# Optimization experiments

Hardware: AMD Instinct MI355X
Metric: run time of the kernel (lower is better)

## Reference

```python
import jax, jax.numpy as jnp
import numpy as np

N_IN = 200000
N_OUT = 600000
K = 27          # 3x3x3 kernel offsets
P = 150000      # kernel-map pairs per offset
C_IN = 96
C_OUT = 96
BN_EPS = 1e-5


def setup_inputs() -> dict:
    key = jax.random.key(0)
    k1, k2, k3, k4 = jax.random.split(key, 4)
    feats = jax.random.normal(k1, (N_IN, C_IN), dtype=jnp.float32)
    # kernel map: per offset, input-site indices and output-site indices
    in_idx = jax.random.randint(k2, (K, P), 0, N_IN, dtype=jnp.int32)
    out_idx = jax.random.randint(k3, (K, P), 0, N_OUT, dtype=jnp.int32)
    weight = jax.random.normal(k4, (K, C_IN, C_OUT), dtype=jnp.float32) * (1.0 / np.sqrt(C_IN * K))
    gamma = jnp.ones((C_OUT,), dtype=jnp.float32)
    beta = jnp.zeros((C_OUT,), dtype=jnp.float32)
    return {"feats": feats, "in_idx": in_idx, "out_idx": out_idx,
            "weight": weight, "gamma": gamma, "beta": beta}


def reference(feats, in_idx, out_idx, weight, gamma, beta):
    # Sparse transposed conv: gather -> matmul -> scatter-add per kernel offset.
    out = jnp.zeros((N_OUT, C_OUT), dtype=feats.dtype)
    for k in range(K):  # fixed small loop over kernel offsets (structurally distinct weights)
        contrib = feats[in_idx[k]] @ weight[k]          # [P, C_OUT]
        out = out.at[out_idx[k]].add(contrib)
    # BatchNorm (training-mode batch stats over active output sites), per channel
    mean = jnp.mean(out, axis=0)
    var = jnp.mean((out - mean) ** 2, axis=0)
    y = (out - mean) * jax.lax.rsqrt(var + BN_EPS) * gamma + beta
    # ReLU
    return jax.nn.relu(y)
```

## Files before the change

kernel.cpp:

```cpp
#include <hip/hip_runtime.h>
#include <hip/hip_bf16.h>

#define N_IN   200000
#define N_OUT  600000
#define KOFF   27
#define PPAIR  150000
#define NPAIR  (KOFF * PPAIR)
#define C      96
#define BN_EPS 1e-5f

using bf16x8 = __attribute__((ext_vector_type(8))) __bf16;
using f32x4  = __attribute__((ext_vector_type(4))) float;

static __device__ __forceinline__ unsigned short f2b(float x) {
    __hip_bfloat16 h = __float2bfloat16(x);
    return *reinterpret_cast<unsigned short*>(&h);
}
static __device__ __forceinline__ float b_lo(unsigned int u) { return __uint_as_float(u << 16); }
static __device__ __forceinline__ float b_hi(unsigned int u) { return __uint_as_float(u & 0xffff0000u); }

__global__ void cvt_feats(const float* __restrict__ src, unsigned short* __restrict__ dst) {
    int t = blockIdx.x * 256 + threadIdx.x;
    const float4* s4 = (const float4*)src;
    float4 a = s4[2 * t], b = s4[2 * t + 1];
    union { unsigned short u[8]; uint4 v; } r;
    r.u[0] = f2b(a.x); r.u[1] = f2b(a.y); r.u[2] = f2b(a.z); r.u[3] = f2b(a.w);
    r.u[4] = f2b(b.x); r.u[5] = f2b(b.y); r.u[6] = f2b(b.z); r.u[7] = f2b(b.w);
    ((uint4*)dst)[t] = r.v;
}

__global__ void cvt_w(const float* __restrict__ w, unsigned short* __restrict__ wt) {
    int t = blockIdx.x * 256 + threadIdx.x;
    int k = t / 9216;
    int rem = t - k * 9216;
    int o = rem / 96;
    int i = rem - o * 96;
    wt[t] = f2b(w[k * 9216 + i * 96 + o]);
}

__global__ void k_hist(const int* __restrict__ out_idx, int* __restrict__ counts,
                       int* __restrict__ lrank) {
    int t = blockIdx.x * 256 + threadIdx.x;
    if (t < NPAIR) lrank[t] = atomicAdd(&counts[out_idx[t]], 1);
}

__global__ void k_bsum(const int* __restrict__ counts, int* __restrict__ bsum) {
    __shared__ int ls[256];
    int b = blockIdx.x, t = threadIdx.x;
    int base = b * 1024 + t * 4;
    int s = 0;
#pragma unroll
    for (int j = 0; j < 4; j++) { int i = base + j; if (i < N_OUT) s += counts[i]; }
    ls[t] = s;
    __syncthreads();
    for (int off = 128; off > 0; off >>= 1) {
        if (t < off) ls[t] += ls[t + off];
        __syncthreads();
    }
    if (t == 0) bsum[b] = ls[0];
}

__global__ void k_scan_bsum(const int* __restrict__ bsum, int* __restrict__ bsum_ex) {
    __shared__ int sc[1024];
    int t = threadIdx.x;
    int v = (t < 586) ? bsum[t] : 0;
    sc[t] = v;
    __syncthreads();
    for (int off = 1; off < 1024; off <<= 1) {
        int add = (t >= off) ? sc[t - off] : 0;
        __syncthreads();
        sc[t] += add;
        __syncthreads();
    }
    bsum_ex[t] = sc[t] - v;
}

__global__ void k_scan_local(const int* __restrict__ counts, const int* __restrict__ bsum_ex,
                             int* __restrict__ csr) {
    __shared__ int sc[256];
    int b = blockIdx.x, t = threadIdx.x;
    int base = b * 1024 + t * 4;
    int c[4];
    int s = 0;
#pragma unroll
    for (int j = 0; j < 4; j++) {
        int i = base + j;
        c[j] = (i < N_OUT) ? counts[i] : 0;
        s += c[j];
    }
    sc[t] = s;
    __syncthreads();
    for (int off = 1; off < 256; off <<= 1) {
        int add = (t >= off) ? sc[t - off] : 0;
        __syncthreads();
        sc[t] += add;
        __syncthreads();
    }
    int run = bsum_ex[b] + sc[t] - s;
#pragma unroll
    for (int j = 0; j < 4; j++) {
        int i = base + j;
        if (i < N_OUT) {
            csr[i] = run;
            run += c[j];
            if (i == N_OUT - 1) csr[N_OUT] = run;
        }
    }
}

__global__ __launch_bounds__(256, 6) void contrib_k(
    const unsigned short* __restrict__ fb,
    const unsigned short* __restrict__ wt,
    const int* __restrict__ in_idx,
    const int* __restrict__ out_idx,
    const int* __restrict__ csr,
    const int* __restrict__ lrank,
    unsigned short* __restrict__ contrib)
{
    __shared__ int s_g[64];
    __shared__ int s_rank[64];

    const int t    = threadIdx.x;
    const int k    = blockIdx.y;
    const int row0 = blockIdx.x * 64;
    const long kp  = (long)k * PPAIR;

    if (t < 64) {
        int p  = row0 + t;
        int pc = (p < PPAIR) ? p : (PPAIR - 1);
        s_g[t]    = in_idx[kp + pc];
        s_rank[t] = (p < PPAIR) ? (csr[out_idx[kp + p]] + lrank[kp + p]) : -1;
    }
    __syncthreads();

    const int wave = t >> 6, lane = t & 63;
    const int quad = lane >> 4, l16 = lane & 15;

    const unsigned short* arow  = fb + (size_t)s_g[wave * 16 + l16] * 96 + quad * 8;
    const unsigned short* bbase = wt + (size_t)k * 9216 + l16 * 96 + quad * 8;

    f32x4 acc[6];
#pragma unroll
    for (int n = 0; n < 6; n++) acc[n] = (f32x4){0.f, 0.f, 0.f, 0.f};

#pragma unroll
    for (int kk = 0; kk < 3; kk++) {
        bf16x8 a = *(const bf16x8*)(arow + kk * 32);
#pragma unroll
        for (int n = 0; n < 6; n++) {
            bf16x8 b = *(const bf16x8*)(bbase + n * 16 * 96 + kk * 32);
            acc[n] = __builtin_amdgcn_mfma_f32_16x16x32_bf16(b, a, acc[n], 0, 0, 0);
        }
    }

    const int rk = s_rank[wave * 16 + l16];
    if (rk >= 0) {
        unsigned short* crow = contrib + (size_t)rk * 96 + quad * 4;
#pragma unroll
        for (int n = 0; n < 6; n++) {
            uint2 v;
            v.x = (unsigned)f2b(acc[n][0]) | ((unsigned)f2b(acc[n][1]) << 16);
            v.y = (unsigned)f2b(acc[n][2]) | ((unsigned)f2b(acc[n][3]) << 16);
            *(uint2*)(crow + n * 16) = v;
        }
    }
}

__global__ __launch_bounds__(384) void reduce_bn(
    const unsigned short* __restrict__ contrib,
    const int* __restrict__ csr,
    float* __restrict__ out,
    float* __restrict__ sums)
{
    __shared__ float lsum[96], lq[96];
    int t = threadIdx.x;
    int rl = t / 24, c4 = t - rl * 24;
    float ps0 = 0.f, ps1 = 0.f, ps2 = 0.f, ps3 = 0.f;
    float pq0 = 0.f, pq1 = 0.f, pq2 = 0.f, pq3 = 0.f;

    for (int rb = blockIdx.x * 16; rb < N_OUT; rb += gridDim.x * 16) {
        int r = rb + rl;
        int s = csr[r], e = csr[r + 1];
        float a0 = 0.f, a1 = 0.f, a2 = 0.f, a3 = 0.f;
        int j = s;
        for (; j + 1 < e; j += 2) {
            uint2 u = *(const uint2*)(contrib + (size_t)j * 96 + c4 * 4);
            uint2 v = *(const uint2*)(contrib + (size_t)(j + 1) * 96 + c4 * 4);
            a0 += b_lo(u.x); a1 += b_hi(u.x); a2 += b_lo(u.y); a3 += b_hi(u.y);
            a0 += b_lo(v.x); a1 += b_hi(v.x); a2 += b_lo(v.y); a3 += b_hi(v.y);
        }
        if (j < e) {
            uint2 u = *(const uint2*)(contrib + (size_t)j * 96 + c4 * 4);
            a0 += b_lo(u.x); a1 += b_hi(u.x); a2 += b_lo(u.y); a3 += b_hi(u.y);
        }
        *(float4*)(out + (size_t)r * 96 + c4 * 4) = make_float4(a0, a1, a2, a3);
        ps0 += a0; ps1 += a1; ps2 += a2; ps3 += a3;
        pq0 += a0 * a0; pq1 += a1 * a1; pq2 += a2 * a2; pq3 += a3 * a3;
    }

    if (t < 96) { lsum[t] = 0.f; lq[t] = 0.f; }
    __syncthreads();
    atomicAdd(&lsum[c4 * 4 + 0], ps0); atomicAdd(&lsum[c4 * 4 + 1], ps1);
    atomicAdd(&lsum[c4 * 4 + 2], ps2); atomicAdd(&lsum[c4 * 4 + 3], ps3);
    atomicAdd(&lq[c4 * 4 + 0], pq0);   atomicAdd(&lq[c4 * 4 + 1], pq1);
    atomicAdd(&lq[c4 * 4 + 2], pq2);   atomicAdd(&lq[c4 * 4 + 3], pq3);
    __syncthreads();
    if (t < 96) {
        atomicAdd(&sums[t], lsum[t]);
        atomicAdd(&sums[96 + t], lq[t]);
    }
}

__global__ void bn_final(float* __restrict__ sums, const float* __restrict__ gamma,
                         const float* __restrict__ beta) {
    int c = threadIdx.x;
    if (c < 96) {
        float mean = sums[c] * (1.0f / (float)N_OUT);
        float var  = sums[96 + c] * (1.0f / (float)N_OUT) - mean * mean;
        float inv  = rsqrtf(var + BN_EPS);
        float sc   = inv * gamma[c];
        sums[c]      = sc;
        sums[96 + c] = beta[c] - mean * sc;
    }
}

__global__ void bn_apply(float* __restrict__ out, const float* __restrict__ sums) {
    int t = blockIdx.x * 256 + threadIdx.x;
    int g = t % 24;
    float sc0 = sums[g * 4 + 0], sc1 = sums[g * 4 + 1];
    float sc2 = sums[g * 4 + 2], sc3 = sums[g * 4 + 3];
    float sh0 = sums[96 + g * 4 + 0], sh1 = sums[96 + g * 4 + 1];
    float sh2 = sums[96 + g * 4 + 2], sh3 = sums[96 + g * 4 + 3];
    float4* o4 = (float4*)out;
    for (long f = t; f < 14400000L; f += 258048) {
        float4 v = o4[f];
        v.x = fmaxf(v.x * sc0 + sh0, 0.f);
        v.y = fmaxf(v.y * sc1 + sh1, 0.f);
        v.z = fmaxf(v.z * sc2 + sh2, 0.f);
        v.w = fmaxf(v.w * sc3 + sh3, 0.f);
        o4[f] = v;
    }
}

extern "C" void kernel_launch(void* const* d_in, const int* in_sizes, int n_in,
                              void* d_out, int out_size, void* d_ws, size_t ws_size,
                              hipStream_t stream) {
    const float* feats  = (const float*)d_in[0];
    const int* in_idx   = (const int*)d_in[1];
    const int* out_idx  = (const int*)d_in[2];
    const float* weight = (const float*)d_in[3];
    const float* gamma  = (const float*)d_in[4];
    const float* beta   = (const float*)d_in[5];
    float* out = (float*)d_out;

    char* ws = (char*)d_ws;
    size_t off = 0;
    unsigned short* fb      = (unsigned short*)(ws + off); off += 38400000;
    unsigned short* wt      = (unsigned short*)(ws + off); off += 497664;
    unsigned short* contrib = (unsigned short*)(ws + off); off += (size_t)NPAIR * 96 * 2;
    int* counts             = (int*)(ws + off); off += 2400000;
    int* csr                = (int*)(ws + off); off += 2400016;
    int* bsum               = (int*)(ws + off); off += 4096;
    int* bsum_ex            = (int*)(ws + off); off += 4096;
    int* lrank              = (int*)(ws + off); off += (size_t)NPAIR * 4;
    float* sums             = (float*)(ws + off); off += 768;

    hipMemsetAsync(counts, 0, (size_t)N_OUT * sizeof(int), stream);
    hipMemsetAsync(sums, 0, 192 * sizeof(float), stream);

    cvt_feats<<<9375, 256, 0, stream>>>(feats, fb);
    cvt_w<<<972, 256, 0, stream>>>(weight, wt);

    k_hist<<<(NPAIR + 255) / 256, 256, 0, stream>>>(out_idx, counts, lrank);
    k_bsum<<<586, 256, 0, stream>>>(counts, bsum);
    k_scan_bsum<<<1, 1024, 0, stream>>>(bsum, bsum_ex);
    k_scan_local<<<586, 256, 0, stream>>>(counts, bsum_ex, csr);

    contrib_k<<<dim3(2344, KOFF), 256, 0, stream>>>(fb, wt, in_idx, out_idx, csr, lrank, contrib);

    reduce_bn<<<9375, 384, 0, stream>>>(contrib, csr, out, sums);
    bn_final<<<1, 128, 0, stream>>>(sums, gamma, beta);
    bn_apply<<<1008, 256, 0, stream>>>(out, sums);
}
```

Baseline: 1.544 ms.

## Shuffle MFMA outputs into 16-byte nontemporal stores and use nontemporal loads

The GEMM epilogue now packs accumulators to bf16 and exchanges them across lanes with shuffles, so each lane writes a contiguous 16-byte chunk of a contrib row with a nontemporal store instead of six scattered 8-byte stores. The reduce and BN-apply kernels use nontemporal loads and stores on streaming data to limit cache pollution. This adds shuffle instructions and may lose L2 reuse if contrib rows are read back while still cached.

```diff
diff --git a/kernel.cpp b/kernel.cpp
--- a/kernel.cpp
+++ b/kernel.cpp
@@ -11,6 +11,7 @@
 
 using bf16x8 = __attribute__((ext_vector_type(8))) __bf16;
 using f32x4  = __attribute__((ext_vector_type(4))) float;
+using u32x4  = __attribute__((ext_vector_type(4))) unsigned int;
 
 static __device__ __forceinline__ unsigned short f2b(float x) {
     __hip_bfloat16 h = __float2bfloat16(x);
@@ -153,15 +154,36 @@
         }
     }
 
-    const int rk = s_rank[wave * 16 + l16];
-    if (rk >= 0) {
-        unsigned short* crow = contrib + (size_t)rk * 96 + quad * 4;
-#pragma unroll
-        for (int n = 0; n < 6; n++) {
-            uint2 v;
-            v.x = (unsigned)f2b(acc[n][0]) | ((unsigned)f2b(acc[n][1]) << 16);
-            v.y = (unsigned)f2b(acc[n][2]) | ((unsigned)f2b(acc[n][3]) << 16);
-            *(uint2*)(crow + n * 16) = v;
+    unsigned int pk[6][2];
+#pragma unroll
+    for (int n = 0; n < 6; n++) {
+        pk[n][0] = (unsigned)f2b(acc[n][0]) | ((unsigned)f2b(acc[n][1]) << 16);
+        pk[n][1] = (unsigned)f2b(acc[n][2]) | ((unsigned)f2b(acc[n][3]) << 16);
+    }
+
+    const int rk   = s_rank[wave * 16 + l16];
+    const int srcA = ((quad & 1) << 5) + l16;
+    const int srcB = srcA + 16;
+    const bool hi  = (quad >> 1) != 0;
+
+#pragma unroll
+    for (int s = 0; s < 3; s++) {
+        unsigned a0 = (unsigned)__shfl((int)pk[2 * s][0], srcA);
+        unsigned a1 = (unsigned)__shfl((int)pk[2 * s][1], srcA);
+        unsigned a2 = (unsigned)__shfl((int)pk[2 * s][0], srcB);
+        unsigned a3 = (unsigned)__shfl((int)pk[2 * s][1], srcB);
+        unsigned b0 = (unsigned)__shfl((int)pk[2 * s + 1][0], srcA);
+        unsigned b1 = (unsigned)__shfl((int)pk[2 * s + 1][1], srcA);
+        unsigned b2 = (unsigned)__shfl((int)pk[2 * s + 1][0], srcB);
+        unsigned b3 = (unsigned)__shfl((int)pk[2 * s + 1][1], srcB);
+        u32x4 v;
+        v.x = hi ? b0 : a0;
+        v.y = hi ? b1 : a1;
+        v.z = hi ? b2 : a2;
+        v.w = hi ? b3 : a3;
+        if (rk >= 0) {
+            __builtin_nontemporal_store(
+                v, (u32x4*)(contrib + (size_t)rk * 96 + s * 32 + quad * 8));
         }
     }
 }
@@ -184,14 +206,20 @@
         float a0 = 0.f, a1 = 0.f, a2 = 0.f, a3 = 0.f;
         int j = s;
         for (; j + 1 < e; j += 2) {
-            uint2 u = *(const uint2*)(contrib + (size_t)j * 96 + c4 * 4);
-            uint2 v = *(const uint2*)(contrib + (size_t)(j + 1) * 96 + c4 * 4);
-            a0 += b_lo(u.x); a1 += b_hi(u.x); a2 += b_lo(u.y); a3 += b_hi(u.y);
-            a0 += b_lo(v.x); a1 += b_hi(v.x); a2 += b_lo(v.y); a3 += b_hi(v.y);
+            unsigned long long u = __builtin_nontemporal_load(
+                (const unsigned long long*)(contrib + (size_t)j * 96 + c4 * 4));
+            unsigned long long v = __builtin_nontemporal_load(
+                (const unsigned long long*)(contrib + (size_t)(j + 1) * 96 + c4 * 4));
+            unsigned ux = (unsigned)u, uy = (unsigned)(u >> 32);
+            unsigned vx = (unsigned)v, vy = (unsigned)(v >> 32);
+            a0 += b_lo(ux); a1 += b_hi(ux); a2 += b_lo(uy); a3 += b_hi(uy);
+            a0 += b_lo(vx); a1 += b_hi(vx); a2 += b_lo(vy); a3 += b_hi(vy);
         }
         if (j < e) {
-            uint2 u = *(const uint2*)(contrib + (size_t)j * 96 + c4 * 4);
-            a0 += b_lo(u.x); a1 += b_hi(u.x); a2 += b_lo(u.y); a3 += b_hi(u.y);
+            unsigned long long u = __builtin_nontemporal_load(
+                (const unsigned long long*)(contrib + (size_t)j * 96 + c4 * 4));
+            unsigned ux = (unsigned)u, uy = (unsigned)(u >> 32);
+            a0 += b_lo(ux); a1 += b_hi(ux); a2 += b_lo(uy); a3 += b_hi(uy);
         }
         *(float4*)(out + (size_t)r * 96 + c4 * 4) = make_float4(a0, a1, a2, a3);
         ps0 += a0; ps1 += a1; ps2 += a2; ps3 += a3;
@@ -231,14 +259,14 @@
     float sc2 = sums[g * 4 + 2], sc3 = sums[g * 4 + 3];
     float sh0 = sums[96 + g * 4 + 0], sh1 = sums[96 + g * 4 + 1];
     float sh2 = sums[96 + g * 4 + 2], sh3 = sums[96 + g * 4 + 3];
-    float4* o4 = (float4*)out;
+    f32x4* o4 = (f32x4*)out;
     for (long f = t; f < 14400000L; f += 258048) {
-        float4 v = o4[f];
+        f32x4 v = __builtin_nontemporal_load(o4 + f);
         v.x = fmaxf(v.x * sc0 + sh0, 0.f);
         v.y = fmaxf(v.y * sc1 + sh1, 0.f);
         v.z = fmaxf(v.z * sc2 + sh2, 0.f);
         v.w = fmaxf(v.w * sc3 + sh3, 0.f);
-        o4[f] = v;
+        __builtin_nontemporal_store(v, o4 + f);
     }
 }
 
```

Result: faster. 1.429 ms (-7.5%).

## Write contributions in pair order and gather via permutation in reduction

Applied to the files above, without the earlier changes.

The matmul kernel now writes each pair's bf16 contribution row at its own pair index, with coalesced nontemporal stores, instead of scattering it to a CSR-sorted slot. A new k_perm kernel builds a pair permutation so reduce_bn gathers rows through perm[j]. The histogram rank is shrunk to one byte and counts are scanned in place inside the csr buffer. Nontemporal hints and raised launch-bounds occupancy are also applied. This moves the random access from the matmul's stores to the reduction's loads, and adds an extra kernel plus an indirection read per pair.

```diff
diff --git a/kernel.cpp b/kernel.cpp
--- a/kernel.cpp
+++ b/kernel.cpp
@@ -11,6 +11,7 @@
 
 using bf16x8 = __attribute__((ext_vector_type(8))) __bf16;
 using f32x4  = __attribute__((ext_vector_type(4))) float;
+using u32x2  = __attribute__((ext_vector_type(2))) unsigned int;
 
 static __device__ __forceinline__ unsigned short f2b(float x) {
     __hip_bfloat16 h = __float2bfloat16(x);
@@ -39,9 +40,9 @@
 }
 
 __global__ void k_hist(const int* __restrict__ out_idx, int* __restrict__ counts,
-                       int* __restrict__ lrank) {
-    int t = blockIdx.x * 256 + threadIdx.x;
-    if (t < NPAIR) lrank[t] = atomicAdd(&counts[out_idx[t]], 1);
+                       unsigned char* __restrict__ lrank) {
+    int t = blockIdx.x * 256 + threadIdx.x;
+    if (t < NPAIR) lrank[t] = (unsigned char)atomicAdd(&counts[out_idx[t]], 1);
 }
 
 __global__ void k_bsum(const int* __restrict__ counts, int* __restrict__ bsum) {
@@ -75,8 +76,7 @@
     bsum_ex[t] = sc[t] - v;
 }
 
-__global__ void k_scan_local(const int* __restrict__ counts, const int* __restrict__ bsum_ex,
-                             int* __restrict__ csr) {
+__global__ void k_scan_local(int* __restrict__ csr, const int* __restrict__ bsum_ex) {
     __shared__ int sc[256];
     int b = blockIdx.x, t = threadIdx.x;
     int base = b * 1024 + t * 4;
@@ -85,7 +85,7 @@
 #pragma unroll
     for (int j = 0; j < 4; j++) {
         int i = base + j;
-        c[j] = (i < N_OUT) ? counts[i] : 0;
+        c[j] = (i < N_OUT) ? csr[i] : 0;
         s += c[j];
     }
     sc[t] = s;
@@ -108,35 +108,31 @@
     }
 }
 
-__global__ __launch_bounds__(256, 6) void contrib_k(
+__global__ void k_perm(const int* __restrict__ out_idx, const unsigned char* __restrict__ lrank,
+                       const int* __restrict__ csr, int* __restrict__ perm) {
+    int t = blockIdx.x * 256 + threadIdx.x;
+    if (t < NPAIR) perm[csr[out_idx[t]] + (int)lrank[t]] = t;
+}
+
+__global__ __launch_bounds__(256, 8) void contrib_k(
     const unsigned short* __restrict__ fb,
     const unsigned short* __restrict__ wt,
     const int* __restrict__ in_idx,
-    const int* __restrict__ out_idx,
-    const int* __restrict__ csr,
-    const int* __restrict__ lrank,
     unsigned short* __restrict__ contrib)
 {
-    __shared__ int s_g[64];
-    __shared__ int s_rank[64];
-
     const int t    = threadIdx.x;
     const int k    = blockIdx.y;
     const int row0 = blockIdx.x * 64;
     const long kp  = (long)k * PPAIR;
 
-    if (t < 64) {
-        int p  = row0 + t;
-        int pc = (p < PPAIR) ? p : (PPAIR - 1);
-        s_g[t]    = in_idx[kp + pc];
-        s_rank[t] = (p < PPAIR) ? (csr[out_idx[kp + p]] + lrank[kp + p]) : -1;
-    }
-    __syncthreads();
-
     const int wave = t >> 6, lane = t & 63;
     const int quad = lane >> 4, l16 = lane & 15;
 
-    const unsigned short* arow  = fb + (size_t)s_g[wave * 16 + l16] * 96 + quad * 8;
+    const int pb = row0 + wave * 16 + l16;
+    const int pc = (pb < PPAIR) ? pb : (PPAIR - 1);
+    const int g  = in_idx[kp + pc];
+
+    const unsigned short* arow  = fb + (size_t)g * 96 + quad * 8;
     const unsigned short* bbase = wt + (size_t)k * 9216 + l16 * 96 + quad * 8;
 
     f32x4 acc[6];
@@ -153,15 +149,14 @@
         }
     }
 
-    const int rk = s_rank[wave * 16 + l16];
-    if (rk >= 0) {
-        unsigned short* crow = contrib + (size_t)rk * 96 + quad * 4;
+    if (pb < PPAIR) {
+        unsigned short* crow = contrib + (size_t)(kp + pb) * 96 + quad * 4;
 #pragma unroll
         for (int n = 0; n < 6; n++) {
-            uint2 v;
+            u32x2 v;
             v.x = (unsigned)f2b(acc[n][0]) | ((unsigned)f2b(acc[n][1]) << 16);
             v.y = (unsigned)f2b(acc[n][2]) | ((unsigned)f2b(acc[n][3]) << 16);
-            *(uint2*)(crow + n * 16) = v;
+            __builtin_nontemporal_store(v, (u32x2*)(crow + n * 16));
         }
     }
 }
@@ -169,6 +164,7 @@
 __global__ __launch_bounds__(384) void reduce_bn(
     const unsigned short* __restrict__ contrib,
     const int* __restrict__ csr,
+    const int* __restrict__ perm,
     float* __restrict__ out,
     float* __restrict__ sums)
 {
@@ -184,14 +180,22 @@
         float a0 = 0.f, a1 = 0.f, a2 = 0.f, a3 = 0.f;
         int j = s;
         for (; j + 1 < e; j += 2) {
-            uint2 u = *(const uint2*)(contrib + (size_t)j * 96 + c4 * 4);
-            uint2 v = *(const uint2*)(contrib + (size_t)(j + 1) * 96 + c4 * 4);
-            a0 += b_lo(u.x); a1 += b_hi(u.x); a2 += b_lo(u.y); a3 += b_hi(u.y);
-            a0 += b_lo(v.x); a1 += b_hi(v.x); a2 += b_lo(v.y); a3 += b_hi(v.y);
+            int p0 = perm[j], p1 = perm[j + 1];
+            unsigned long long u = __builtin_nontemporal_load(
+                (const unsigned long long*)(contrib + (size_t)p0 * 96 + c4 * 4));
+            unsigned long long v = __builtin_nontemporal_load(
+                (const unsigned long long*)(contrib + (size_t)p1 * 96 + c4 * 4));
+            unsigned ux = (unsigned)u, uy = (unsigned)(u >> 32);
+            unsigned vx = (unsigned)v, vy = (unsigned)(v >> 32);
+            a0 += b_lo(ux); a1 += b_hi(ux); a2 += b_lo(uy); a3 += b_hi(uy);
+            a0 += b_lo(vx); a1 += b_hi(vx); a2 += b_lo(vy); a3 += b_hi(vy);
         }
         if (j < e) {
-            uint2 u = *(const uint2*)(contrib + (size_t)j * 96 + c4 * 4);
-            a0 += b_lo(u.x); a1 += b_hi(u.x); a2 += b_lo(u.y); a3 += b_hi(u.y);
+            int p0 = perm[j];
+            unsigned long long u = __builtin_nontemporal_load(
+                (const unsigned long long*)(contrib + (size_t)p0 * 96 + c4 * 4));
+            unsigned ux = (unsigned)u, uy = (unsigned)(u >> 32);
+            a0 += b_lo(ux); a1 += b_hi(ux); a2 += b_lo(uy); a3 += b_hi(uy);
         }
         *(float4*)(out + (size_t)r * 96 + c4 * 4) = make_float4(a0, a1, a2, a3);
         ps0 += a0; ps1 += a1; ps2 += a2; ps3 += a3;
@@ -231,14 +235,14 @@
     float sc2 = sums[g * 4 + 2], sc3 = sums[g * 4 + 3];
     float sh0 = sums[96 + g * 4 + 0], sh1 = sums[96 + g * 4 + 1];
     float sh2 = sums[96 + g * 4 + 2], sh3 = sums[96 + g * 4 + 3];
-    float4* o4 = (float4*)out;
+    f32x4* o4 = (f32x4*)out;
     for (long f = t; f < 14400000L; f += 258048) {
-        float4 v = o4[f];
+        f32x4 v = __builtin_nontemporal_load(o4 + f);
         v.x = fmaxf(v.x * sc0 + sh0, 0.f);
         v.y = fmaxf(v.y * sc1 + sh1, 0.f);
         v.z = fmaxf(v.z * sc2 + sh2, 0.f);
         v.w = fmaxf(v.w * sc3 + sh3, 0.f);
-        o4[f] = v;
+        __builtin_nontemporal_store(v, o4 + f);
     }
 }
 
@@ -258,27 +262,28 @@
     unsigned short* fb      = (unsigned short*)(ws + off); off += 38400000;
     unsigned short* wt      = (unsigned short*)(ws + off); off += 497664;
     unsigned short* contrib = (unsigned short*)(ws + off); off += (size_t)NPAIR * 96 * 2;
-    int* counts             = (int*)(ws + off); off += 2400000;
     int* csr                = (int*)(ws + off); off += 2400016;
     int* bsum               = (int*)(ws + off); off += 4096;
     int* bsum_ex            = (int*)(ws + off); off += 4096;
-    int* lrank              = (int*)(ws + off); off += (size_t)NPAIR * 4;
+    unsigned char* lrank    = (unsigned char*)(ws + off); off += NPAIR;
+    int* perm               = (int*)(ws + off); off += (size_t)NPAIR * 4;
     float* sums             = (float*)(ws + off); off += 768;
 
-    hipMemsetAsync(counts, 0, (size_t)N_OUT * sizeof(int), stream);
+    hipMemsetAsync(csr, 0, (size_t)N_OUT * sizeof(int), stream);
     hipMemsetAsync(sums, 0, 192 * sizeof(float), stream);
 
     cvt_feats<<<9375, 256, 0, stream>>>(feats, fb);
     cvt_w<<<972, 256, 0, stream>>>(weight, wt);
 
-    k_hist<<<(NPAIR + 255) / 256, 256, 0, stream>>>(out_idx, counts, lrank);
-    k_bsum<<<586, 256, 0, stream>>>(counts, bsum);
+    k_hist<<<(NPAIR + 255) / 256, 256, 0, stream>>>(out_idx, csr, lrank);
+    k_bsum<<<586, 256, 0, stream>>>(csr, bsum);
     k_scan_bsum<<<1, 1024, 0, stream>>>(bsum, bsum_ex);
-    k_scan_local<<<586, 256, 0, stream>>>(counts, bsum_ex, csr);
-
-    contrib_k<<<dim3(2344, KOFF), 256, 0, stream>>>(fb, wt, in_idx, out_idx, csr, lrank, contrib);
-
-    reduce_bn<<<9375, 384, 0, stream>>>(contrib, csr, out, sums);
+    k_scan_local<<<586, 256, 0, stream>>>(csr, bsum_ex);
+    k_perm<<<(NPAIR + 255) / 256, 256, 0, stream>>>(out_idx, lrank, csr, perm);
+
+    contrib_k<<<dim3(2344, KOFF), 256, 0, stream>>>(fb, wt, in_idx, contrib);
+
+    reduce_bn<<<9375, 384, 0, stream>>>(contrib, csr, perm, out, sums);
     bn_final<<<1, 128, 0, stream>>>(sums, gamma, beta);
     bn_apply<<<1008, 256, 0, stream>>>(out, sums);
 }
```

Result: slower. 1.596 ms (+3.4%).
